# Kernel tuning notes

Measured on AMD Instinct MI355X. Metric: run time of the kernel, lower is better.

## Reference

```python
import jax, jax.numpy as jnp
import numpy as np

N, E = 50000, 800000
IN, HID, OUT, H = 128, 16, 16, 4


def setup_inputs() -> dict:
    key = jax.random.key(0)
    ks = jax.random.split(key, 11)
    sc = 0.1
    return {
        "features": jax.random.normal(ks[0], (N, IN), jnp.float32),
        "src": jax.random.randint(ks[1], (E,), 0, N, dtype=jnp.int64) if jax.config.jax_enable_x64 else jax.random.randint(ks[1], (E,), 0, N).astype(jnp.int32),
        "dst": jax.random.randint(ks[2], (E,), 0, N).astype(jnp.int32),
        "W1": jax.random.normal(ks[3], (H * HID, IN), jnp.float32) * sc,
        "al1": jax.random.normal(ks[4], (H, HID), jnp.float32) * sc,
        "ar1": jax.random.normal(ks[5], (H, HID), jnp.float32) * sc,
        "b1": jax.random.normal(ks[6], (H * HID,), jnp.float32) * sc,
        "W2": jax.random.normal(ks[7], (H * OUT, H * HID), jnp.float32) * sc,
        "al2": jax.random.normal(ks[8], (H, OUT), jnp.float32) * sc,
        "ar2": jax.random.normal(ks[9], (H, OUT), jnp.float32) * sc,
        "b2": jax.random.normal(ks[10], (H * OUT,), jnp.float32) * sc,
    }


def gat_conv(src, dst, feat, W, al, ar, b, heads, dout):
    """DGL-style GATConv: fc -> edge attention -> dst-softmax -> scatter-sum."""
    n = feat.shape[0]
    h = (feat @ W.T).reshape(n, heads, dout)            # [N,H,D]
    el = jnp.einsum("nhd,hd->nh", h, al)                # [N,H]
    er = jnp.einsum("nhd,hd->nh", h, ar)                # [N,H]
    e = jax.nn.leaky_relu(el[src] + er[dst], 0.2)       # [E,H]
    m = jax.ops.segment_max(e, dst, num_segments=n)     # per-dst max, [N,H]
    a = jnp.exp(e - m[dst])                             # [E,H]
    s = jax.ops.segment_sum(a, dst, num_segments=n)     # [N,H]
    alpha = a / s[dst]                                  # edge softmax, [E,H]
    out = jax.ops.segment_sum(alpha[:, :, None] * h[src], dst, num_segments=n)
    return out + b.reshape(1, heads, dout)              # [N,H,D]


def reference(features, src, dst, W1, al1, ar1, b1, W2, al2, ar2, b2):
    h = gat_conv(src, dst, features, W1, al1, ar1, b1, H, HID).reshape(N, H * HID)
    h = jax.nn.relu(h)
    h = gat_conv(src, dst, h, W2, al2, ar2, b2, H, OUT).mean(axis=1)  # mean over heads
    return jax.nn.log_softmax(h, axis=1)
```

## Files before the change

### kernel.cpp

```cpp
#include <hip/hip_runtime.h>
#include <math.h>

#define N_NODES 50000
#define N_EDGES 800000
#define NPART 8
#define PART_SZ ((N_NODES + NPART - 1) / NPART)
#define CAP 64
#define SCAT_BLOCKS 4096
#define FC_BLOCKS 784

typedef __attribute__((ext_vector_type(8))) short short8;
typedef __attribute__((ext_vector_type(8))) unsigned short ushort8;
typedef __attribute__((ext_vector_type(4))) float v4f;
typedef __attribute__((ext_vector_type(2))) float v2f;
typedef __attribute__((ext_vector_type(4))) int int4v;

__device__ __forceinline__ unsigned short f2bf(float f) {
    unsigned int u = __float_as_uint(f);
    u += 0x7fff + ((u >> 16) & 1);
    return (unsigned short)(u >> 16);
}

__device__ __forceinline__ short8 load_afrag(const float* X, size_t row, int K,
                                             int kc, int quad) {
    const float* p = X + row * K + kc * 32 + quad * 8;
    const float4 t0 = *(const float4*)p;
    const float4 t1 = *(const float4*)(p + 4);
    short8 a;
    a[0] = (short)f2bf(t0.x); a[1] = (short)f2bf(t0.y);
    a[2] = (short)f2bf(t0.z); a[3] = (short)f2bf(t0.w);
    a[4] = (short)f2bf(t1.x); a[5] = (short)f2bf(t1.y);
    a[6] = (short)f2bf(t1.z); a[7] = (short)f2bf(t1.w);
    return a;
}

template <int K, typename XT>
__device__ __forceinline__ void fc_att_body(
    const XT* __restrict__ X, const float* __restrict__ W,
    const float* __restrict__ al, const float* __restrict__ ar,
    unsigned short* __restrict__ Hout, float* __restrict__ el,
    float* __restrict__ er, int nTiles, int blk, unsigned short* Wlds)
{
    constexpr int KP = K + 8;
    constexpr int NKC = K / 32;
    const int tid = threadIdx.x;
    for (int i = tid; i < 64 * K; i += 256) {
        const int r = i / K, c = i - r * K;
        Wlds[r * KP + c] = f2bf(W[i]);
    }
    __syncthreads();

    const int lane = tid & 63;
    const int wave = tid >> 6;
    const int d = lane & 15;
    const int quad = lane >> 4;

    const int tile = blk * 4 + wave;
    if (tile >= nTiles) return;
    const int node0 = tile * 16;

    short8 wf[4][NKC];
#pragma unroll
    for (int ng = 0; ng < 4; ++ng) {
#pragma unroll
        for (int kc = 0; kc < NKC; ++kc) {
            wf[ng][kc] = *(const short8*)&Wlds[(ng * 16 + d) * KP + kc * 32 + quad * 8];
        }
    }

    v4f cc[4] = {{0.f,0.f,0.f,0.f},{0.f,0.f,0.f,0.f},{0.f,0.f,0.f,0.f},{0.f,0.f,0.f,0.f}};
#pragma unroll
    for (int kc = 0; kc < NKC; ++kc) {
        const short8 a = load_afrag(X, (size_t)(node0 + d), K, kc, quad);
        cc[0] = __builtin_amdgcn_mfma_f32_16x16x32_bf16(a, wf[0][kc], cc[0], 0, 0, 0);
        cc[1] = __builtin_amdgcn_mfma_f32_16x16x32_bf16(a, wf[1][kc], cc[1], 0, 0, 0);
        cc[2] = __builtin_amdgcn_mfma_f32_16x16x32_bf16(a, wf[2][kc], cc[2], 0, 0, 0);
        cc[3] = __builtin_amdgcn_mfma_f32_16x16x32_bf16(a, wf[3][kc], cc[3], 0, 0, 0);
    }

#pragma unroll
    for (int ng = 0; ng < 4; ++ng) {
        const float alv = al[ng * 16 + d];
        const float arv = ar[ng * 16 + d];
        const v4f c = cc[ng];
#pragma unroll
        for (int r = 0; r < 4; ++r) {
            const int node = node0 + quad * 4 + r;
            Hout[(size_t)node * 64 + ng * 16 + d] = f2bf(c[r]);
            float vel = c[r] * alv;
            float ver = c[r] * arv;
#pragma unroll
            for (int off = 1; off < 16; off <<= 1) {
                vel += __shfl_xor(vel, off);
                ver += __shfl_xor(ver, off);
            }
            if (d == 0) {
                el[node * 4 + ng] = vel;
                er[node * 4 + ng] = ver;
            }
        }
    }
}

__global__ __launch_bounds__(256) void l1_fused_kernel(
    const float* __restrict__ X, const float* __restrict__ W,
    const float* __restrict__ al, const float* __restrict__ ar,
    unsigned short* __restrict__ Hout, float* __restrict__ el,
    float* __restrict__ er,
    const int* __restrict__ src, const int* __restrict__ dst,
    int* __restrict__ cnt16, unsigned short* __restrict__ col)
{
    __shared__ __align__(16) unsigned short Wlds[64 * (128 + 8)];
    if ((int)blockIdx.x < FC_BLOCKS) {
        fc_att_body<128, float>(X, W, al, ar, Hout, el, er,
                                N_NODES / 16, (int)blockIdx.x, Wlds);
    } else {
        const int bid = (int)blockIdx.x - FC_BLOCKS;
        const int part = bid & (NPART - 1);
        const int lo = part * PART_SZ;
        const int hi = lo + PART_SZ;
        const int tid_p = (bid >> 3) * 256 + (int)threadIdx.x;
        const int stride = (SCAT_BLOCKS / NPART) * 256;
        const int4v* dst4 = (const int4v*)dst;
        const int4v* src4 = (const int4v*)src;
        const int NQ = N_EDGES / 4;
        for (int q = tid_p; q < NQ; q += 2 * stride) {
            const int q2 = q + stride;
            const bool ok2 = q2 < NQ;
            const int4v dA = __builtin_nontemporal_load(dst4 + q);
            const int4v sA = __builtin_nontemporal_load(src4 + q);
            const int4v dB = ok2 ? __builtin_nontemporal_load(dst4 + q2) : (int4v){-1,-1,-1,-1};
            const int4v sB = ok2 ? __builtin_nontemporal_load(src4 + q2) : (int4v){0,0,0,0};
            const int dd[8] = {dA[0], dA[1], dA[2], dA[3], dB[0], dB[1], dB[2], dB[3]};
            const int ss[8] = {sA[0], sA[1], sA[2], sA[3], sB[0], sB[1], sB[2], sB[3]};
            int pos[8];
#pragma unroll
            for (int j = 0; j < 8; ++j) {
                pos[j] = -1;
                if (dd[j] >= lo && dd[j] < hi)
                    pos[j] = atomicAdd(&cnt16[(unsigned)dd[j] * 16], 1);
            }
#pragma unroll
            for (int j = 0; j < 8; ++j) {
                if (pos[j] >= 0 && pos[j] < CAP)
                    col[(unsigned)dd[j] * CAP + pos[j]] = (unsigned short)ss[j];
            }
        }
    }
}

template <int ELS>
__device__ __forceinline__ void agg_iter16(
    const unsigned short* __restrict__ colrow, int i, int rm,
    const float* __restrict__ el, const unsigned int* __restrict__ Hf32,
    int hb, int hl, int j_a, unsigned h_a, int hd, float erv_a,
    float& accL0, float& accL1, float& accH0, float& accH1, float& sacc_a)
{
    const ushort8 sv0 = __builtin_nontemporal_load((const ushort8*)(colrow + i));
    const ushort8 sv1 = __builtin_nontemporal_load((const ushort8*)(colrow + i + 8));
    const unsigned sa0 = (unsigned)colrow[i + j_a];
    const unsigned sa1 = (unsigned)colrow[i + 8 + j_a];
    float x0 = el[sa0 * ELS + h_a] + erv_a;
    float x1 = el[sa1 * ELS + h_a] + erv_a;
    x0 = fmaxf(x0, 0.2f * x0);
    x1 = fmaxf(x1, 0.2f * x1);
    float a0 = __expf(x0);
    float a1 = __expf(x1);
    a0 = (j_a < rm) ? a0 : 0.f;
    a1 = (j_a + 8 < rm) ? a1 : 0.f;
    sacc_a += a0 + a1;
    unsigned uu[16];
#pragma unroll
    for (int j = 0; j < 8; ++j)
        uu[j] = Hf32[(unsigned)sv0[j] * 32u + (unsigned)hl];
#pragma unroll
    for (int j = 0; j < 8; ++j)
        uu[8 + j] = Hf32[(unsigned)sv1[j] * 32u + (unsigned)hl];
#pragma unroll
    for (int j = 0; j < 8; ++j) {
        const float aj = __shfl(a0, hb + j * 4 + hd);
        const float lo = __uint_as_float(uu[j] << 16);
        const float hi = __uint_as_float(uu[j] & 0xffff0000u);
        if (j & 1) { accL1 = fmaf(aj, lo, accL1); accH1 = fmaf(aj, hi, accH1); }
        else       { accL0 = fmaf(aj, lo, accL0); accH0 = fmaf(aj, hi, accH0); }
    }
#pragma unroll
    for (int j = 0; j < 8; ++j) {
        const float aj = __shfl(a1, hb + j * 4 + hd);
        const float lo = __uint_as_float(uu[8 + j] << 16);
        const float hi = __uint_as_float(uu[8 + j] & 0xffff0000u);
        if (j & 1) { accL1 = fmaf(aj, lo, accL1); accH1 = fmaf(aj, hi, accH1); }
        else       { accL0 = fmaf(aj, lo, accL0); accH0 = fmaf(aj, hi, accH0); }
    }
}

template <int ELS>
__device__ __forceinline__ void agg_walk_pair(
    const unsigned short* __restrict__ colrow, int len, int len_max,
    const float* __restrict__ el, const unsigned int* __restrict__ Hf32,
    int hb, int hl, float erv_a,
    float& accL_out, float& accH_out, float& sacc_a_out)
{
    const int j_a = hl >> 2;
    const unsigned h_a = (unsigned)(hl & 3);
    const int hd = hl >> 3;
    float accL0 = 0.f, accL1 = 0.f, accH0 = 0.f, accH1 = 0.f;
    float sacc_a = 0.f;
    agg_iter16<ELS>(colrow, 0, len, el, Hf32, hb, hl, j_a, h_a, hd, erv_a,
                    accL0, accL1, accH0, accH1, sacc_a);
    for (int i = 16; i < len_max; i += 16)
        agg_iter16<ELS>(colrow, i, len - i, el, Hf32, hb, hl, j_a, h_a, hd,
                        erv_a, accL0, accL1, accH0, accH1, sacc_a);
    sacc_a += __shfl_xor(sacc_a, 4);
    sacc_a += __shfl_xor(sacc_a, 8);
    sacc_a += __shfl_xor(sacc_a, 16);
    sacc_a_out = sacc_a;
    accL_out = accL0 + accL1;
    accH_out = accH0 + accH1;
}

__global__ __launch_bounds__(512) void agg1_fc2_fused(
    const int* __restrict__ cnt16, const unsigned short* __restrict__ col,
    const float* __restrict__ el1, const float* __restrict__ er1,
    const unsigned int* __restrict__ H1, const float* __restrict__ b1,
    const float* __restrict__ W2, const float* __restrict__ al2,
    const float* __restrict__ ar2,
    unsigned short* __restrict__ H2,
    float* __restrict__ el2, float* __restrict__ er2)
{
    __shared__ __align__(16) unsigned short W2lds[64 * 72];
    __shared__ __align__(16) unsigned int Hlds[16 * 33];

    const int tid = threadIdx.x;
    const int lane = tid & 63;
    const int wave = tid >> 6;
    const int hl = lane & 31;
    const int hb = lane & 32;
    const int nl = wave * 2 + (lane >> 5);
    const int node = (int)blockIdx.x * 16 + nl;
    const int hd = hl >> 3;
    const int cg = hd * 16 + (hl & 7) * 2;

    const int len = min(cnt16[(unsigned)node * 16], CAP);
    const float erv_a = er1[node * 4 + (hl & 3)];
    const float bL = b1[cg];
    const float bH = b1[cg + 1];

    for (int i = tid; i < 64 * 64; i += 512) {
        const int r = i >> 6, c = i & 63;
        W2lds[r * 72 + c] = f2bf(W2[i]);
    }

    const int len_max = max(len, __shfl_xor(len, 32));
    float accL, accH, sacc_a;
    agg_walk_pair<4>(col + (unsigned)node * CAP, len, len_max, el1, H1,
                     hb, hl, erv_a, accL, accH, sacc_a);
    const float sc = __shfl(sacc_a, hb + hd);
    float vL = sc > 0.f ? accL / sc : 0.f;
    float vH = sc > 0.f ? accH / sc : 0.f;
    vL += bL;  vH += bH;
    vL = vL > 0.f ? vL : 0.f;
    vH = vH > 0.f ? vH : 0.f;
    Hlds[nl * 33 + hl] = (unsigned)f2bf(vL) | ((unsigned)f2bf(vH) << 16);
    __syncthreads();
    if (wave >= 4) return;

    const int ng = wave;
    const int d = lane & 15;
    const int quad = lane >> 4;
    const unsigned short* lds16 = (const unsigned short*)Hlds;
    const short8 wf0 = *(const short8*)&W2lds[(ng * 16 + d) * 72 + quad * 8];
    const short8 wf1 = *(const short8*)&W2lds[(ng * 16 + d) * 72 + 32 + quad * 8];
    const short8 a0 = *(const short8*)&lds16[(unsigned)d * 66 + quad * 8];
    const short8 a1 = *(const short8*)&lds16[(unsigned)d * 66 + 32 + quad * 8];
    v4f c0 = {0.f, 0.f, 0.f, 0.f};
    c0 = __builtin_amdgcn_mfma_f32_16x16x32_bf16(a0, wf0, c0, 0, 0, 0);
    c0 = __builtin_amdgcn_mfma_f32_16x16x32_bf16(a1, wf1, c0, 0, 0, 0);

    const float alv = al2[ng * 16 + d];
    const float arv = ar2[ng * 16 + d];
#pragma unroll
    for (int r = 0; r < 4; ++r) {
        const int node2 = (int)blockIdx.x * 16 + quad * 4 + r;
        H2[(size_t)node2 * 64 + ng * 16 + d] = f2bf(c0[r]);
        float vel = c0[r] * alv;
        float ver = c0[r] * arv;
#pragma unroll
        for (int off = 1; off < 16; off <<= 1) {
            vel += __shfl_xor(vel, off);
            ver += __shfl_xor(ver, off);
        }
        if (d == 0) {
            el2[node2 * 16 + ng] = vel;
            er2[node2 * 16 + ng] = ver;
        }
    }
}

__global__ __launch_bounds__(256) void agg_final_kernel(
    const int* __restrict__ cnt16, const unsigned short* __restrict__ col,
    const float* __restrict__ el2, const float* __restrict__ er2,
    const unsigned int* __restrict__ Hf32, const float* __restrict__ b,
    float* __restrict__ out, int n)
{
    const int lane = threadIdx.x & 63;
    const int wave = threadIdx.x >> 6;
    const int hl = lane & 31;
    const int hb = lane & 32;
    const int node = blockIdx.x * 8 + wave * 2 + (lane >> 5);
    if (node >= n) return;
    const int hd = hl >> 3;
    const int cg = hd * 16 + (hl & 7) * 2;
    const float erv_a = er2[node * 16 + (hl & 3)];
    const float bL = b[cg];
    const float bH = b[cg + 1];
    const int len = min(cnt16[(unsigned)node * 16], CAP);
    const int len_max = max(len, __shfl_xor(len, 32));
    float accL, accH, sacc_a;
    agg_walk_pair<16>(col + (unsigned)node * CAP, len, len_max, el2, Hf32,
                      hb, hl, erv_a, accL, accH, sacc_a);
    const float sc = __shfl(sacc_a, hb + hd);
    float zL = sc > 0.f ? accL / sc : 0.f;
    float zH = sc > 0.f ? accH / sc : 0.f;
    zL += bL;   zH += bH;
    zL += __shfl_xor(zL, 8);  zL += __shfl_xor(zL, 16);  zL *= 0.25f;
    zH += __shfl_xor(zH, 8);  zH += __shfl_xor(zH, 16);  zH *= 0.25f;
    float m = fmaxf(zL, zH);
    m = fmaxf(m, __shfl_xor(m, 1));
    m = fmaxf(m, __shfl_xor(m, 2));
    m = fmaxf(m, __shfl_xor(m, 4));
    float se = __expf(zL - m) + __expf(zH - m);
    se += __shfl_xor(se, 1);
    se += __shfl_xor(se, 2);
    se += __shfl_xor(se, 4);
    const float lse = __logf(se);
    if (hl < 8) {
        v2f r;
        r[0] = zL - m - lse;
        r[1] = zH - m - lse;
        __builtin_nontemporal_store(r, (v2f*)(out + (size_t)node * 16 + hl * 2));
    }
}

extern "C" void kernel_launch(void* const* d_in, const int* in_sizes, int n_in,
                              void* d_out, int out_size, void* d_ws, size_t ws_size,
                              hipStream_t stream)
{
    const float* feat = (const float*)d_in[0];
    const int*   src  = (const int*)d_in[1];
    const int*   dst  = (const int*)d_in[2];
    const float* W1   = (const float*)d_in[3];
    const float* al1  = (const float*)d_in[4];
    const float* ar1  = (const float*)d_in[5];
    const float* b1   = (const float*)d_in[6];
    const float* W2   = (const float*)d_in[7];
    const float* al2  = (const float*)d_in[8];
    const float* ar2  = (const float*)d_in[9];
    const float* b2   = (const float*)d_in[10];
    float* out = (float*)d_out;

    float* el1 = (float*)d_ws;
    float* er1 = el1 + N_NODES * 4;
    int*   cnt16 = (int*)(er1 + N_NODES * 4);
    uintptr_t p = ((uintptr_t)(cnt16 + N_NODES * 16) + 15) & ~(uintptr_t)15;
    unsigned short* col = (unsigned short*)p;
    unsigned short* A   = col + (size_t)N_NODES * CAP + 64;
    unsigned short* B   = A + (size_t)N_NODES * 64;
    float* el2 = (float*)cnt16 + 4;
    float* er2 = (float*)cnt16 + 8;

    const int AB2 = (N_NODES + 7) / 8;
    const int TILES = N_NODES / 16;

    (void)hipMemsetAsync(cnt16, 0, (size_t)((char*)A - (char*)cnt16), stream);

    l1_fused_kernel<<<FC_BLOCKS + SCAT_BLOCKS, 256, 0, stream>>>(
        feat, W1, al1, ar1, A, el1, er1, src, dst, cnt16, col);

    agg1_fc2_fused<<<TILES, 512, 0, stream>>>(
        cnt16, col, el1, er1, (const unsigned int*)A, b1,
        W2, al2, ar2, B, el2, er2);

    agg_final_kernel<<<AB2, 256, 0, stream>>>(cnt16, col, el2, er2,
                                              (const unsigned int*)B, b2,
                                              out, N_NODES);
}
```

Baseline: 179.6 us.

## Merge layer-2 aggregation into persistent cooperative kernel with grid sync and prefetch

Replaces the separate agg1_fc2 and agg_final launches with one persistent cooperative kernel. It loops over tiles, runs a grid-wide sync, then does the final aggregation and log-softmax. This removes a kernel launch boundary, and W2 goes to LDS once per block instead of once per tile. The edge walk is also software-pipelined: the next chunk's col indices and el values are loaded before the current chunk is consumed, to hide gather latency. The trade-offs are grid-sync overhead, reduced parallelism from the persistent grid size, and extra register pressure from the prefetch.

```diff
diff --git a/kernel.cpp b/kernel.cpp
--- a/kernel.cpp
+++ b/kernel.cpp
@@ -1,5 +1,8 @@
 #include <hip/hip_runtime.h>
+#include <hip/hip_cooperative_groups.h>
 #include <math.h>
+
+namespace cg = cooperative_groups;
 
 #define N_NODES 50000
 #define N_EDGES 800000
@@ -8,6 +11,7 @@
 #define CAP 64
 #define SCAT_BLOCKS 4096
 #define FC_BLOCKS 784
+#define TILES (N_NODES / 16)
 
 typedef __attribute__((ext_vector_type(8))) short short8;
 typedef __attribute__((ext_vector_type(8))) unsigned short ushort8;
@@ -113,7 +117,7 @@
     __shared__ __align__(16) unsigned short Wlds[64 * (128 + 8)];
     if ((int)blockIdx.x < FC_BLOCKS) {
         fc_att_body<128, float>(X, W, al, ar, Hout, el, er,
-                                N_NODES / 16, (int)blockIdx.x, Wlds);
+                                TILES, (int)blockIdx.x, Wlds);
     } else {
         const int bid = (int)blockIdx.x - FC_BLOCKS;
         const int part = bid & (NPART - 1);
@@ -149,19 +153,28 @@
     }
 }
 
+struct AggPre { ushort8 sv0, sv1; float e0, e1; };
+
 template <int ELS>
-__device__ __forceinline__ void agg_iter16(
-    const unsigned short* __restrict__ colrow, int i, int rm,
-    const float* __restrict__ el, const unsigned int* __restrict__ Hf32,
-    int hb, int hl, int j_a, unsigned h_a, int hd, float erv_a,
+__device__ __forceinline__ AggPre agg_issue(
+    const unsigned short* __restrict__ colrow, int i,
+    const float* __restrict__ el, int j_a, unsigned h_a)
+{
+    AggPre p;
+    p.sv0 = __builtin_nontemporal_load((const ushort8*)(colrow + i));
+    p.sv1 = __builtin_nontemporal_load((const ushort8*)(colrow + i + 8));
+    p.e0 = el[(unsigned)colrow[i + j_a] * ELS + h_a];
+    p.e1 = el[(unsigned)colrow[i + 8 + j_a] * ELS + h_a];
+    return p;
+}
+
+__device__ __forceinline__ void agg_consume(
+    const AggPre& p, int rm, const unsigned int* __restrict__ Hf32,
+    int hb, int hl, int j_a, int hd, float erv_a,
     float& accL0, float& accL1, float& accH0, float& accH1, float& sacc_a)
 {
-    const ushort8 sv0 = __builtin_nontemporal_load((const ushort8*)(colrow + i));
-    const ushort8 sv1 = __builtin_nontemporal_load((const ushort8*)(colrow + i + 8));
-    const unsigned sa0 = (unsigned)colrow[i + j_a];
-    const unsigned sa1 = (unsigned)colrow[i + 8 + j_a];
-    float x0 = el[sa0 * ELS + h_a] + erv_a;
-    float x1 = el[sa1 * ELS + h_a] + erv_a;
+    float x0 = p.e0 + erv_a;
+    float x1 = p.e1 + erv_a;
     x0 = fmaxf(x0, 0.2f * x0);
     x1 = fmaxf(x1, 0.2f * x1);
     float a0 = __expf(x0);
@@ -172,10 +185,10 @@
     unsigned uu[16];
 #pragma unroll
     for (int j = 0; j < 8; ++j)
-        uu[j] = Hf32[(unsigned)sv0[j] * 32u + (unsigned)hl];
+        uu[j] = Hf32[(unsigned)p.sv0[j] * 32u + (unsigned)hl];
 #pragma unroll
     for (int j = 0; j < 8; ++j)
-        uu[8 + j] = Hf32[(unsigned)sv1[j] * 32u + (unsigned)hl];
+        uu[8 + j] = Hf32[(unsigned)p.sv1[j] * 32u + (unsigned)hl];
 #pragma unroll
     for (int j = 0; j < 8; ++j) {
         const float aj = __shfl(a0, hb + j * 4 + hd);
@@ -196,7 +209,7 @@
 
 template <int ELS>
 __device__ __forceinline__ void agg_walk_pair(
-    const unsigned short* __restrict__ colrow, int len, int len_max,
+    const unsigned short* __restrict__ colrow, int len,
     const float* __restrict__ el, const unsigned int* __restrict__ Hf32,
     int hb, int hl, float erv_a,
     float& accL_out, float& accH_out, float& sacc_a_out)
@@ -204,13 +217,16 @@
     const int j_a = hl >> 2;
     const unsigned h_a = (unsigned)(hl & 3);
     const int hd = hl >> 3;
-    float accL0 = 0.f, accL1 = 0.f, accH0 = 0.f, accH1 = 0.f;
-    float sacc_a = 0.f;
-    agg_iter16<ELS>(colrow, 0, len, el, Hf32, hb, hl, j_a, h_a, hd, erv_a,
+    float accL0 = 0.f, accL1 = 0.f, accH0 = 0.f, accH1 = 0.f, sacc_a = 0.f;
+    AggPre p = agg_issue<ELS>(colrow, 0, el, j_a, h_a);
+    const int len_max = max(len, __shfl_xor(len, 32));
+    for (int i = 0; i < len_max; i += 16) {
+        const int inx = (i + 16 < len_max) ? i + 16 : 0;
+        AggPre np = agg_issue<ELS>(colrow, inx, el, j_a, h_a);
+        agg_consume(p, len - i, Hf32, hb, hl, j_a, hd, erv_a,
                     accL0, accL1, accH0, accH1, sacc_a);
-    for (int i = 16; i < len_max; i += 16)
-        agg_iter16<ELS>(colrow, i, len - i, el, Hf32, hb, hl, j_a, h_a, hd,
-                        erv_a, accL0, accL1, accH0, accH1, sacc_a);
+        p = np;
+    }
     sacc_a += __shfl_xor(sacc_a, 4);
     sacc_a += __shfl_xor(sacc_a, 8);
     sacc_a += __shfl_xor(sacc_a, 16);
@@ -219,14 +235,14 @@
     accH_out = accH0 + accH1;
 }
 
-__global__ __launch_bounds__(512) void agg1_fc2_fused(
+__global__ __launch_bounds__(512) void agg_merged(
     const int* __restrict__ cnt16, const unsigned short* __restrict__ col,
     const float* __restrict__ el1, const float* __restrict__ er1,
     const unsigned int* __restrict__ H1, const float* __restrict__ b1,
     const float* __restrict__ W2, const float* __restrict__ al2,
-    const float* __restrict__ ar2,
-    unsigned short* __restrict__ H2,
-    float* __restrict__ el2, float* __restrict__ er2)
+    const float* __restrict__ ar2, unsigned short* __restrict__ H2,
+    float* __restrict__ el2, float* __restrict__ er2,
+    const float* __restrict__ b2, float* __restrict__ out)
 {
     __shared__ __align__(16) unsigned short W2lds[64 * 72];
     __shared__ __align__(16) unsigned int Hlds[16 * 33];
@@ -237,108 +253,103 @@
     const int hl = lane & 31;
     const int hb = lane & 32;
     const int nl = wave * 2 + (lane >> 5);
-    const int node = (int)blockIdx.x * 16 + nl;
     const int hd = hl >> 3;
-    const int cg = hd * 16 + (hl & 7) * 2;
-
-    const int len = min(cnt16[(unsigned)node * 16], CAP);
-    const float erv_a = er1[node * 4 + (hl & 3)];
-    const float bL = b1[cg];
-    const float bH = b1[cg + 1];
+    const int cgp = hd * 16 + (hl & 7) * 2;
 
     for (int i = tid; i < 64 * 64; i += 512) {
         const int r = i >> 6, c = i & 63;
         W2lds[r * 72 + c] = f2bf(W2[i]);
     }
-
-    const int len_max = max(len, __shfl_xor(len, 32));
-    float accL, accH, sacc_a;
-    agg_walk_pair<4>(col + (unsigned)node * CAP, len, len_max, el1, H1,
-                     hb, hl, erv_a, accL, accH, sacc_a);
-    const float sc = __shfl(sacc_a, hb + hd);
-    float vL = sc > 0.f ? accL / sc : 0.f;
-    float vH = sc > 0.f ? accH / sc : 0.f;
-    vL += bL;  vH += bH;
-    vL = vL > 0.f ? vL : 0.f;
-    vH = vH > 0.f ? vH : 0.f;
-    Hlds[nl * 33 + hl] = (unsigned)f2bf(vL) | ((unsigned)f2bf(vH) << 16);
+    const float bL1 = b1[cgp];
+    const float bH1 = b1[cgp + 1];
     __syncthreads();
-    if (wave >= 4) return;
-
-    const int ng = wave;
+
     const int d = lane & 15;
     const int quad = lane >> 4;
-    const unsigned short* lds16 = (const unsigned short*)Hlds;
-    const short8 wf0 = *(const short8*)&W2lds[(ng * 16 + d) * 72 + quad * 8];
-    const short8 wf1 = *(const short8*)&W2lds[(ng * 16 + d) * 72 + 32 + quad * 8];
-    const short8 a0 = *(const short8*)&lds16[(unsigned)d * 66 + quad * 8];
-    const short8 a1 = *(const short8*)&lds16[(unsigned)d * 66 + 32 + quad * 8];
-    v4f c0 = {0.f, 0.f, 0.f, 0.f};
-    c0 = __builtin_amdgcn_mfma_f32_16x16x32_bf16(a0, wf0, c0, 0, 0, 0);
-    c0 = __builtin_amdgcn_mfma_f32_16x16x32_bf16(a1, wf1, c0, 0, 0, 0);
-
-    const float alv = al2[ng * 16 + d];
-    const float arv = ar2[ng * 16 + d];
-#pragma unroll
-    for (int r = 0; r < 4; ++r) {
-        const int node2 = (int)blockIdx.x * 16 + quad * 4 + r;
-        H2[(size_t)node2 * 64 + ng * 16 + d] = f2bf(c0[r]);
-        float vel = c0[r] * alv;
-        float ver = c0[r] * arv;
-#pragma unroll
-        for (int off = 1; off < 16; off <<= 1) {
-            vel += __shfl_xor(vel, off);
-            ver += __shfl_xor(ver, off);
+    short8 wf0{}, wf1{};
+    float alv = 0.f, arv = 0.f;
+    if (wave < 4) {
+        wf0 = *(const short8*)&W2lds[(wave * 16 + d) * 72 + quad * 8];
+        wf1 = *(const short8*)&W2lds[(wave * 16 + d) * 72 + 32 + quad * 8];
+        alv = al2[wave * 16 + d];
+        arv = ar2[wave * 16 + d];
+    }
+
+    for (int tile = (int)blockIdx.x; tile < TILES; tile += (int)gridDim.x) {
+        const int node = tile * 16 + nl;
+        const int len = min(cnt16[(unsigned)node * 16], CAP);
+        const float erv_a = er1[node * 4 + (hl & 3)];
+        float accL, accH, sacc_a;
+        agg_walk_pair<4>(col + (unsigned)node * CAP, len, el1, H1,
+                         hb, hl, erv_a, accL, accH, sacc_a);
+        const float sc = __shfl(sacc_a, hb + hd);
+        float vL = sc > 0.f ? accL / sc : 0.f;
+        float vH = sc > 0.f ? accH / sc : 0.f;
+        vL += bL1;  vH += bH1;
+        vL = vL > 0.f ? vL : 0.f;
+        vH = vH > 0.f ? vH : 0.f;
+        Hlds[nl * 33 + hl] = (unsigned)f2bf(vL) | ((unsigned)f2bf(vH) << 16);
+        __syncthreads();
+        if (wave < 4) {
+            const unsigned short* lds16 = (const unsigned short*)Hlds;
+            const short8 a0 = *(const short8*)&lds16[(unsigned)d * 66 + quad * 8];
+            const short8 a1 = *(const short8*)&lds16[(unsigned)d * 66 + 32 + quad * 8];
+            v4f c0 = {0.f, 0.f, 0.f, 0.f};
+            c0 = __builtin_amdgcn_mfma_f32_16x16x32_bf16(a0, wf0, c0, 0, 0, 0);
+            c0 = __builtin_amdgcn_mfma_f32_16x16x32_bf16(a1, wf1, c0, 0, 0, 0);
+#pragma unroll
+            for (int r = 0; r < 4; ++r) {
+                const int node2 = tile * 16 + quad * 4 + r;
+                H2[(size_t)node2 * 64 + wave * 16 + d] = f2bf(c0[r]);
+                float vel = c0[r] * alv;
+                float ver = c0[r] * arv;
+#pragma unroll
+                for (int off = 1; off < 16; off <<= 1) {
+                    vel += __shfl_xor(vel, off);
+                    ver += __shfl_xor(ver, off);
+                }
+                if (d == 0) {
+                    el2[node2 * 16 + wave] = vel;
+                    er2[node2 * 16 + wave] = ver;
+                }
+            }
         }
-        if (d == 0) {
-            el2[node2 * 16 + ng] = vel;
-            er2[node2 * 16 + ng] = ver;
+        __syncthreads();
+    }
+
+    cg::this_grid().sync();
+
+    const float bL2 = b2[cgp];
+    const float bH2 = b2[cgp + 1];
+    for (int chunk = (int)blockIdx.x; chunk < TILES; chunk += (int)gridDim.x) {
+        const int node = chunk * 16 + nl;
+        const float erv_a = er2[node * 16 + (hl & 3)];
+        const int len = min(cnt16[(unsigned)node * 16], CAP);
+        float accL, accH, sacc_a;
+        agg_walk_pair<16>(col + (unsigned)node * CAP, len, el2,
+                          (const unsigned int*)H2, hb, hl, erv_a,
+                          accL, accH, sacc_a);
+        const float sc = __shfl(sacc_a, hb + hd);
+        float zL = sc > 0.f ? accL / sc : 0.f;
+        float zH = sc > 0.f ? accH / sc : 0.f;
+        zL += bL2;   zH += bH2;
+        zL += __shfl_xor(zL, 8);  zL += __shfl_xor(zL, 16);  zL *= 0.25f;
+        zH += __shfl_xor(zH, 8);  zH += __shfl_xor(zH, 16);  zH *= 0.25f;
+        float m = fmaxf(zL, zH);
+        m = fmaxf(m, __shfl_xor(m, 1));
+        m = fmaxf(m, __shfl_xor(m, 2));
+        m = fmaxf(m, __shfl_xor(m, 4));
+        float se = __expf(zL - m) + __expf(zH - m);
+        se += __shfl_xor(se, 1);
+        se += __shfl_xor(se, 2);
+        se += __shfl_xor(se, 4);
+        const float lse = __logf(se);
+        if (hl < 8) {
+            v2f r;
+            r[0] = zL - m - lse;
+            r[1] = zH - m - lse;
+            __builtin_nontemporal_store(r, (v2f*)(out + (size_t)node * 16 + hl * 2));
         }
-    }
-}
-
-__global__ __launch_bounds__(256) void agg_final_kernel(
-    const int* __restrict__ cnt16, const unsigned short* __restrict__ col,
-    const float* __restrict__ el2, const float* __restrict__ er2,
-    const unsigned int* __restrict__ Hf32, const float* __restrict__ b,
-    float* __restrict__ out, int n)
-{
-    const int lane = threadIdx.x & 63;
-    const int wave = threadIdx.x >> 6;
-    const int hl = lane & 31;
-    const int hb = lane & 32;
-    const int node = blockIdx.x * 8 + wave * 2 + (lane >> 5);
-    if (node >= n) return;
-    const int hd = hl >> 3;
-    const int cg = hd * 16 + (hl & 7) * 2;
-    const float erv_a = er2[node * 16 + (hl & 3)];
-    const float bL = b[cg];
-    const float bH = b[cg + 1];
-    const int len = min(cnt16[(unsigned)node * 16], CAP);
-    const int len_max = max(len, __shfl_xor(len, 32));
-    float accL, accH, sacc_a;
-    agg_walk_pair<16>(col + (unsigned)node * CAP, len, len_max, el2, Hf32,
-                      hb, hl, erv_a, accL, accH, sacc_a);
-    const float sc = __shfl(sacc_a, hb + hd);
-    float zL = sc > 0.f ? accL / sc : 0.f;
-    float zH = sc > 0.f ? accH / sc : 0.f;
-    zL += bL;   zH += bH;
-    zL += __shfl_xor(zL, 8);  zL += __shfl_xor(zL, 16);  zL *= 0.25f;
-    zH += __shfl_xor(zH, 8);  zH += __shfl_xor(zH, 16);  zH *= 0.25f;
-    float m = fmaxf(zL, zH);
-    m = fmaxf(m, __shfl_xor(m, 1));
-    m = fmaxf(m, __shfl_xor(m, 2));
-    m = fmaxf(m, __shfl_xor(m, 4));
-    float se = __expf(zL - m) + __expf(zH - m);
-    se += __shfl_xor(se, 1);
-    se += __shfl_xor(se, 2);
-    se += __shfl_xor(se, 4);
-    const float lse = __logf(se);
-    if (hl < 8) {
-        v2f r;
-        r[0] = zL - m - lse;
-        r[1] = zH - m - lse;
-        __builtin_nontemporal_store(r, (v2f*)(out + (size_t)node * 16 + hl * 2));
     }
 }
 
@@ -369,19 +380,30 @@
     float* el2 = (float*)cnt16 + 4;
     float* er2 = (float*)cnt16 + 8;
 
-    const int AB2 = (N_NODES + 7) / 8;
-    const int TILES = N_NODES / 16;
-
     (void)hipMemsetAsync(cnt16, 0, (size_t)((char*)A - (char*)cnt16), stream);
 
     l1_fused_kernel<<<FC_BLOCKS + SCAT_BLOCKS, 256, 0, stream>>>(
         feat, W1, al1, ar1, A, el1, er1, src, dst, cnt16, col);
 
-    agg1_fc2_fused<<<TILES, 512, 0, stream>>>(
-        cnt16, col, el1, er1, (const unsigned int*)A, b1,
-        W2, al2, ar2, B, el2, er2);
-
-    agg_final_kernel<<<AB2, 256, 0, stream>>>(cnt16, col, el2, er2,
-                                              (const unsigned int*)B, b2,
-                                              out, N_NODES);
-}
+    static int coop_grid = 0;
+    if (coop_grid == 0) {
+        int bpc = 0;
+        (void)hipOccupancyMaxActiveBlocksPerMultiprocessor(&bpc, agg_merged, 512, 0);
+        if (bpc < 1) bpc = 1;
+        coop_grid = bpc * 256;
+        if (coop_grid > TILES) coop_grid = TILES;
+    }
+    const int* cnt16c = cnt16;
+    const unsigned short* colc = col;
+    const float *el1c = el1, *er1c = er1, *b1c = b1, *W2c = W2,
+                *al2c = al2, *ar2c = ar2, *b2c = b2;
+    const unsigned int* H1c = (const unsigned int*)A;
+    unsigned short* H2c = B;
+    float *el2c = el2, *er2c = er2, *outc = out;
+    void* args[] = { (void*)&cnt16c, (void*)&colc, (void*)&el1c, (void*)&er1c,
+                     (void*)&H1c, (void*)&b1c, (void*)&W2c, (void*)&al2c,
+                     (void*)&ar2c, (void*)&H2c, (void*)&el2c, (void*)&er2c,
+                     (void*)&b2c, (void*)&outc };
+    (void)hipLaunchCooperativeKernel((const void*)agg_merged, dim3(coop_grid),
+                                     dim3(512), args, 0, stream);
+}
```

Measured after the change: 276.0 us. 1.54x slower.

## Bucket nodes by degree class and process them in permuted order

Applied to the files above, without the earlier changes.

Adds a classify kernel that bins each destination node into one of four degree classes (by 16-edge chunks), and a permute kernel that builds a node permutation grouped by class. Both aggregation kernels then walk nodes through this permutation, so paired half-waves and blocks handle nodes of similar degree. This reduces divergence from the len_max loop across lane pairs and evens out block work. The cost is two extra kernel launches, an indirect node lookup, scattered writes of H2/el2/er2 and output, and worse locality in per-node reads.

```diff
diff --git a/kernel.cpp b/kernel.cpp
--- a/kernel.cpp
+++ b/kernel.cpp
@@ -8,6 +8,7 @@
 #define CAP 64
 #define SCAT_BLOCKS 4096
 #define FC_BLOCKS 784
+#define TILES (N_NODES / 16)
 
 typedef __attribute__((ext_vector_type(8))) short short8;
 typedef __attribute__((ext_vector_type(8))) unsigned short ushort8;
@@ -113,7 +114,7 @@
     __shared__ __align__(16) unsigned short Wlds[64 * (128 + 8)];
     if ((int)blockIdx.x < FC_BLOCKS) {
         fc_att_body<128, float>(X, W, al, ar, Hout, el, er,
-                                N_NODES / 16, (int)blockIdx.x, Wlds);
+                                TILES, (int)blockIdx.x, Wlds);
     } else {
         const int bid = (int)blockIdx.x - FC_BLOCKS;
         const int part = bid & (NPART - 1);
@@ -149,6 +150,44 @@
     }
 }
 
+__global__ __launch_bounds__(256) void classify_kernel(
+    const int* __restrict__ cnt16, unsigned int* __restrict__ pos32,
+    int* __restrict__ classCnt)
+{
+    __shared__ int h[4];
+    __shared__ int base[4];
+    const int tid = threadIdx.x;
+    if (tid < 4) h[tid] = 0;
+    __syncthreads();
+    const int n = (int)blockIdx.x * 256 + tid;
+    int c = 0, r = 0;
+    const bool valid = n < N_NODES;
+    if (valid) {
+        const int len = min(cnt16[(unsigned)n * 16], CAP);
+        c = (len <= 16) ? 0 : (len <= 32) ? 1 : (len <= 48) ? 2 : 3;
+        r = atomicAdd(&h[c], 1);
+    }
+    __syncthreads();
+    if (tid < 4) base[tid] = atomicAdd(&classCnt[tid], h[tid]);
+    __syncthreads();
+    if (valid) pos32[n] = ((unsigned)c << 24) | (unsigned)(base[c] + r);
+}
+
+__global__ __launch_bounds__(256) void permute_kernel(
+    const unsigned int* __restrict__ pos32, const int* __restrict__ classCnt,
+    unsigned short* __restrict__ perm)
+{
+    const int n = (int)blockIdx.x * 256 + (int)threadIdx.x;
+    if (n >= N_NODES) return;
+    const unsigned u = pos32[n];
+    const int c = (int)(u >> 24);
+    const int s = (int)(u & 0xffffffu);
+    const int b0 = classCnt[0], b1 = classCnt[1], b2 = classCnt[2];
+    const int base = (c == 0) ? 0 : (c == 1) ? b0 : (c == 2) ? b0 + b1
+                                                             : b0 + b1 + b2;
+    perm[base + s] = (unsigned short)n;
+}
+
 template <int ELS>
 __device__ __forceinline__ void agg_iter16(
     const unsigned short* __restrict__ colrow, int i, int rm,
@@ -220,6 +259,7 @@
 }
 
 __global__ __launch_bounds__(512) void agg1_fc2_fused(
+    const unsigned short* __restrict__ perm,
     const int* __restrict__ cnt16, const unsigned short* __restrict__ col,
     const float* __restrict__ el1, const float* __restrict__ er1,
     const unsigned int* __restrict__ H1, const float* __restrict__ b1,
@@ -237,7 +277,7 @@
     const int hl = lane & 31;
     const int hb = lane & 32;
     const int nl = wave * 2 + (lane >> 5);
-    const int node = (int)blockIdx.x * 16 + nl;
+    const int node = perm[(unsigned)blockIdx.x * 16 + nl];
     const int hd = hl >> 3;
     const int cg = hd * 16 + (hl & 7) * 2;
 
@@ -281,7 +321,7 @@
     const float arv = ar2[ng * 16 + d];
 #pragma unroll
     for (int r = 0; r < 4; ++r) {
-        const int node2 = (int)blockIdx.x * 16 + quad * 4 + r;
+        const int node2 = perm[(unsigned)blockIdx.x * 16 + quad * 4 + r];
         H2[(size_t)node2 * 64 + ng * 16 + d] = f2bf(c0[r]);
         float vel = c0[r] * alv;
         float ver = c0[r] * arv;
@@ -298,6 +338,7 @@
 }
 
 __global__ __launch_bounds__(256) void agg_final_kernel(
+    const unsigned short* __restrict__ perm,
     const int* __restrict__ cnt16, const unsigned short* __restrict__ col,
     const float* __restrict__ el2, const float* __restrict__ er2,
     const unsigned int* __restrict__ Hf32, const float* __restrict__ b,
@@ -307,8 +348,9 @@
     const int wave = threadIdx.x >> 6;
     const int hl = lane & 31;
     const int hb = lane & 32;
-    const int node = blockIdx.x * 8 + wave * 2 + (lane >> 5);
-    if (node >= n) return;
+    const int idx = blockIdx.x * 8 + wave * 2 + (lane >> 5);
+    if (idx >= n) return;
+    const int node = perm[idx];
     const int hd = hl >> 3;
     const int cg = hd * 16 + (hl & 7) * 2;
     const float erv_a = er2[node * 16 + (hl & 3)];
@@ -364,24 +406,31 @@
     int*   cnt16 = (int*)(er1 + N_NODES * 4);
     uintptr_t p = ((uintptr_t)(cnt16 + N_NODES * 16) + 15) & ~(uintptr_t)15;
     unsigned short* col = (unsigned short*)p;
-    unsigned short* A   = col + (size_t)N_NODES * CAP + 64;
-    unsigned short* B   = A + (size_t)N_NODES * 64;
+    int* classCnt = (int*)(col + (size_t)N_NODES * CAP + 64);
+    unsigned int* pos32 = (unsigned int*)(classCnt + 8);
+    unsigned short* perm = (unsigned short*)(pos32 + N_NODES);
+    uintptr_t pa = ((uintptr_t)(perm + N_NODES) + 15) & ~(uintptr_t)15;
+    unsigned short* A = (unsigned short*)pa;
+    unsigned short* B = A + (size_t)N_NODES * 64;
     float* el2 = (float*)cnt16 + 4;
     float* er2 = (float*)cnt16 + 8;
 
     const int AB2 = (N_NODES + 7) / 8;
-    const int TILES = N_NODES / 16;
+    const int CB  = (N_NODES + 255) / 256;
 
     (void)hipMemsetAsync(cnt16, 0, (size_t)((char*)A - (char*)cnt16), stream);
 
     l1_fused_kernel<<<FC_BLOCKS + SCAT_BLOCKS, 256, 0, stream>>>(
         feat, W1, al1, ar1, A, el1, er1, src, dst, cnt16, col);
 
+    classify_kernel<<<CB, 256, 0, stream>>>(cnt16, pos32, classCnt);
+    permute_kernel<<<CB, 256, 0, stream>>>(pos32, classCnt, perm);
+
     agg1_fc2_fused<<<TILES, 512, 0, stream>>>(
-        cnt16, col, el1, er1, (const unsigned int*)A, b1,
+        perm, cnt16, col, el1, er1, (const unsigned int*)A, b1,
         W2, al2, ar2, B, el2, er2);
 
-    agg_final_kernel<<<AB2, 256, 0, stream>>>(cnt16, col, el2, er2,
+    agg_final_kernel<<<AB2, 256, 0, stream>>>(perm, cnt16, col, el2, er2,
                                               (const unsigned int*)B, b2,
                                               out, N_NODES);
 }
```

New measurement: 187.6 us. +4.4%, slower.
